# Optimization experiments

Hardware: AMD Instinct MI355X
Metric: run time of the kernel (lower is better)

The kernel has to match this reference:

```python
import jax, jax.numpy as jnp
from jax import lax
import numpy as np

B, C, FH, FW, H, V, L = 256, 512, 8, 16, 512, 64, 24


def setup_inputs() -> dict:
    key = jax.random.key(0)
    ks = jax.random.split(key, 32)
    s = 0.05
    n = lambda k, shp: jax.random.normal(k, shp, dtype=jnp.float32) * s
    return {
        "encoder_ftrs": jax.random.normal(ks[0], (B, C, FH, FW), dtype=jnp.float32),
        "sequences": jax.random.randint(ks[1], (B, L), 0, V),
        "test": 0,
        "embed_w": n(ks[2], (V, H)),
        "init_state": n(ks[3], (2, 1, H)),
        "attn_W_w": n(ks[4], (H, C)), "attn_W_b": jnp.zeros((H,), jnp.float32),
        "attn_U_w": n(ks[5], (H, H)), "attn_U_b": jnp.zeros((H,), jnp.float32),
        "attn_v_w": n(ks[6], (1, H)), "attn_v_b": jnp.zeros((1,), jnp.float32),
        "fc_w": n(ks[7], (H, C + H)), "fc_b": jnp.zeros((H,), jnp.float32),
        "cls_w": n(ks[8], (V, H)), "cls_b": jnp.zeros((V,), jnp.float32),
        "gru0_wih": n(ks[9], (3 * H, 2 * H)), "gru0_whh": n(ks[10], (3 * H, H)),
        "gru0_bih": jnp.zeros((3 * H,), jnp.float32), "gru0_bhh": jnp.zeros((3 * H,), jnp.float32),
        "gru1_wih": n(ks[11], (3 * H, H)), "gru1_whh": n(ks[12], (3 * H, H)),
        "gru1_bih": jnp.zeros((3 * H,), jnp.float32), "gru1_bhh": jnp.zeros((3 * H,), jnp.float32),
    }


def _gru_cell(x, h, wih, whh, bih, bhh):
    # PyTorch GRUCell: r,z gates then candidate n with r applied on hidden path
    gi = x @ wih.T + bih
    gh = h @ whh.T + bhh
    i_r, i_z, i_n = jnp.split(gi, 3, axis=-1)
    h_r, h_z, h_n = jnp.split(gh, 3, axis=-1)
    r = jax.nn.sigmoid(i_r + h_r)
    z = jax.nn.sigmoid(i_z + h_z)
    nact = jnp.tanh(i_n + r * h_n)
    return (1.0 - z) * nact + z * h


def reference(encoder_ftrs, sequences, test, embed_w, init_state,
              attn_W_w, attn_W_b, attn_U_w, attn_U_b, attn_v_w, attn_v_b,
              fc_w, fc_b, cls_w, cls_b,
              gru0_wih, gru0_whh, gru0_bih, gru0_bhh,
              gru1_wih, gru1_whh, gru1_bih, gru1_bhh):
    bsz = encoder_ftrs.shape[0]
    # [B, L_sp, C] encoder states
    states = encoder_ftrs.reshape(bsz, C, -1).transpose(0, 2, 1)
    # attn_W(states) is timestep-independent: precompute once (same math)
    Ws = states @ attn_W_w.T + attn_W_b  # [B, L_sp, H]

    def apply_attn(h_top):
        e = jax.nn.relu(Ws + (h_top @ attn_U_w.T + attn_U_b)[:, None, :])
        scores = e @ attn_v_w[0] + attn_v_b[0]          # [B, L_sp]
        a = jax.nn.softmax(scores, axis=-1)
        ctx = jnp.einsum('bl,blc->bc', a, states)        # [B, C]
        return ctx

    def out_proj(ctx, h_top):
        return jax.nn.relu(jnp.concatenate([ctx, h_top], axis=-1) @ fc_w.T + fc_b)

    xs = embed_w[sequences[:, :-1]]                      # [B, T, H]
    h0 = jnp.broadcast_to(init_state, (2, bsz, H))       # repeat over batch
    y0 = out_proj(apply_attn(h0[1]), h0[1])              # time_step == -1 (output dropped)

    def step(carry, x_t):
        h, y = carry
        h_l0 = _gru_cell(jnp.concatenate([y, x_t], axis=-1), h[0],
                         gru0_wih, gru0_whh, gru0_bih, gru0_bhh)
        h_l1 = _gru_cell(h_l0, h[1], gru1_wih, gru1_whh, gru1_bih, gru1_bhh)
        hn = jnp.stack([h_l0, h_l1], axis=0)
        yn = out_proj(apply_attn(h_l1), h_l1)
        return (hn, yn), yn

    _, ys = lax.scan(step, (h0, y0), xs.transpose(1, 0, 2))   # [T, B, H]
    logits = ys.transpose(1, 0, 2) @ cls_w.T + cls_b          # [B, T, V]

    labels = sequences[:, 1:]
    mask = (labels > 0).astype(logits.dtype)
    logp = jax.nn.log_softmax(logits, axis=-1)
    nll = -jnp.take_along_axis(logp, labels[..., None], axis=-1)[..., 0]
    loss = jnp.sum(nll * mask) / jnp.sum(mask)
    return loss
```

## Files before the change

kernel.cpp:

```cpp
#include <hip/hip_runtime.h>
#include <hip/hip_bf16.h>
#include <cstddef>

#define BB 256
#define CC 512
#define SS 128
#define HH 512
#define VV 64
#define LL 24

typedef unsigned short ush;
typedef __attribute__((ext_vector_type(8))) short short8;
typedef __attribute__((ext_vector_type(4))) float f32x4;

__device__ __forceinline__ float wave_sum(float v) {
#pragma unroll
    for (int off = 32; off > 0; off >>= 1) v += __shfl_xor(v, off);
    return v;
}
__device__ __forceinline__ float wave_max(float v) {
#pragma unroll
    for (int off = 32; off > 0; off >>= 1) v = fmaxf(v, __shfl_xor(v, off));
    return v;
}
__device__ __forceinline__ float sigm(float x) { return 1.0f / (1.0f + expf(-x)); }
__device__ __forceinline__ ush f2bf(float f) {
    unsigned u = __float_as_uint(f);
    u += 0x7FFFu + ((u >> 16) & 1u);
    return (ush)(u >> 16);
}
__device__ __forceinline__ float bf2f(ush b) {
    return __uint_as_float(((unsigned)b) << 16);
}
__device__ __forceinline__ unsigned pack2(float a, float b) {
    return (unsigned)f2bf(a) | ((unsigned)f2bf(b) << 16);
}

__global__ __launch_bounds__(256) void init_kernel(const float* __restrict__ init_state,
                                                   float* __restrict__ h0,
                                                   float* __restrict__ h1,
                                                   ush* __restrict__ h0b,
                                                   ush* __restrict__ h1b,
                                                   float* __restrict__ acc) {
    int idx = blockIdx.x * 256 + threadIdx.x;
    if (idx < BB * HH) {
        float a = init_state[idx & (HH - 1)];
        float b = init_state[HH + (idx & (HH - 1))];
        h0[idx] = a; h1[idx] = b;
        h0b[idx] = f2bf(a); h1b[idx] = f2bf(b);
    }
    if (idx < 2) acc[idx] = 0.0f;
}

__global__ __launch_bounds__(256) void conv_kernel(const float* __restrict__ src,
                                                   ush* __restrict__ dst, int n4) {
    int i = blockIdx.x * 256 + threadIdx.x;
    if (i < n4) {
        float4 v = ((const float4*)src)[i];
        uint2 o;
        o.x = pack2(v.x, v.y);
        o.y = pack2(v.z, v.w);
        ((uint2*)dst)[i] = o;
    }
}

__global__ __launch_bounds__(128) void gather_kernel(const float* __restrict__ embed_w,
                                                     const int* __restrict__ seq,
                                                     ush* __restrict__ xall) {
    int item = blockIdx.x;
    int t = item >> 8, m = item & 255;
    int row = seq[m * LL + t];
    float4 v = ((const float4*)(embed_w + (size_t)row * HH))[threadIdx.x];
    uint2 o;
    o.x = pack2(v.x, v.y);
    o.y = pack2(v.z, v.w);
    ((uint2*)(xall + (size_t)item * HH))[threadIdx.x] = o;
}

__global__ __launch_bounds__(256) void enc_conv(const float* __restrict__ enc,
                                                ush* __restrict__ enc_t) {
    int b = blockIdx.x, cg = blockIdx.y;
    int c0 = cg * 128;
    __shared__ ush tile[128][130];
    const float* src = enc + ((size_t)b * 512 + c0) * 128;
#pragma unroll
    for (int i = 0; i < 16; i++) {
        int lin = i * 256 + threadIdx.x;
        int cl = lin >> 5, s4 = lin & 31;
        float4 v = ((const float4*)(src + (size_t)cl * 128))[s4];
        ush b0 = f2bf(v.x), b1 = f2bf(v.y), b2 = f2bf(v.z), b3 = f2bf(v.w);
        tile[s4 * 4 + 0][cl] = b0;
        tile[s4 * 4 + 1][cl] = b1;
        tile[s4 * 4 + 2][cl] = b2;
        tile[s4 * 4 + 3][cl] = b3;
    }
    __syncthreads();
#pragma unroll
    for (int i = 0; i < 16; i++) {
        int lin = i * 256 + threadIdx.x;
        int sl = lin >> 5, c4 = lin & 31;
        ush a0 = tile[sl][c4 * 4 + 0], a1 = tile[sl][c4 * 4 + 1];
        ush a2 = tile[sl][c4 * 4 + 2], a3 = tile[sl][c4 * 4 + 3];
        uint2 o;
        o.x = (unsigned)a0 | ((unsigned)a1 << 16);
        o.y = (unsigned)a2 | ((unsigned)a3 << 16);
        ((uint2*)(enc_t + ((size_t)b * 128 + sl) * 512 + c0))[c4] = o;
    }
}

__global__ __launch_bounds__(256) void ws_v2(const ush* __restrict__ enc_t,
                                             const ush* __restrict__ Wb,
                                             const float* __restrict__ bias,
                                             ush* __restrict__ Ws_bf) {
    int tid = threadIdx.x;
    int wave = tid >> 6, lane = tid & 63;
    int quad = lane >> 4, l16 = lane & 15;
    int m0 = blockIdx.x * 128 + wave * 32;
    int n0 = blockIdx.y * 128;
    const ush* ap = enc_t + (size_t)(m0 + l16) * 512 + quad * 8;
    const ush* bp = Wb + (size_t)(n0 + l16) * 512 + quad * 8;
    f32x4 acc[2][8];
#pragma unroll
    for (int f = 0; f < 2; f++)
#pragma unroll
        for (int s = 0; s < 8; s++) acc[f][s] = (f32x4){0.f, 0.f, 0.f, 0.f};
    short8 ac[2], bc[8], an[2], bn[8];
    ac[0] = *(const short8*)(ap);
    ac[1] = *(const short8*)(ap + (size_t)16 * 512);
#pragma unroll
    for (int s = 0; s < 8; s++) bc[s] = *(const short8*)(bp + (size_t)s * 16 * 512);
#pragma unroll
    for (int ks = 0; ks < 16; ks++) {
        if (ks < 15) {
            int k = (ks + 1) * 32;
            an[0] = *(const short8*)(ap + k);
            an[1] = *(const short8*)(ap + (size_t)16 * 512 + k);
#pragma unroll
            for (int s = 0; s < 8; s++)
                bn[s] = *(const short8*)(bp + (size_t)s * 16 * 512 + k);
        }
#pragma unroll
        for (int f = 0; f < 2; f++)
#pragma unroll
            for (int s = 0; s < 8; s++)
                acc[f][s] = __builtin_amdgcn_mfma_f32_16x16x32_bf16(ac[f], bc[s], acc[f][s], 0, 0, 0);
        if (ks < 15) {
            ac[0] = an[0]; ac[1] = an[1];
#pragma unroll
            for (int s = 0; s < 8; s++) bc[s] = bn[s];
        }
    }
#pragma unroll
    for (int s = 0; s < 8; s++) {
        int n = n0 + s * 16 + l16;
        float bs = bias[n];
#pragma unroll
        for (int f = 0; f < 2; f++)
#pragma unroll
            for (int r = 0; r < 4; r++) {
                int m = m0 + f * 16 + quad * 4 + r;
                Ws_bf[(size_t)m * HH + n] = f2bf(acc[f][s][r] + bs);
            }
    }
}

template <int NSTEP>
__device__ __forceinline__ void segk(const ush* __restrict__ ap,
                                     const ush* __restrict__ bp,
                                     size_t wofs, f32x4& a0, f32x4& a1) {
    short8 as[4], bs0[4], bs1[4];
    constexpr int PRE = NSTEP < 4 ? NSTEP : 4;
#pragma unroll
    for (int i = 0; i < PRE; i++) {
        as[i]  = *(const short8*)(ap + 32 * i);
        bs0[i] = *(const short8*)(bp + 32 * i);
        bs1[i] = *(const short8*)(bp + wofs + 32 * i);
    }
#pragma unroll
    for (int i = 0; i < NSTEP; i++) {
        const int sl = i & 3;
        a0 = __builtin_amdgcn_mfma_f32_16x16x32_bf16(as[sl], bs0[sl], a0, 0, 0, 0);
        a1 = __builtin_amdgcn_mfma_f32_16x16x32_bf16(as[sl], bs1[sl], a1, 0, 0, 0);
        if (i + 4 < NSTEP) {
            as[sl]  = *(const short8*)(ap + 32 * (i + 4));
            bs0[sl] = *(const short8*)(bp + 32 * (i + 4));
            bs1[sl] = *(const short8*)(bp + wofs + 32 * (i + 4));
        }
    }
}

struct GruArgs {
    const ush* xs[8][2];
    const ush* wb[8][2];
    int wst[8][2];
    int nks[8][2];
    int slot[8][2];
    int zmask;
};

__global__ __launch_bounds__(512) void gru_fused(GruArgs A,
                                                 const float* __restrict__ h_prev,
                                                 const float* __restrict__ bih,
                                                 const float* __restrict__ bhh,
                                                 float* __restrict__ h_out,
                                                 ush* __restrict__ h_out_bf) {
    int tid = threadIdx.x;
    int wave = __builtin_amdgcn_readfirstlane(tid >> 6);
    int lane = tid & 63, quad = lane >> 4, l16 = lane & 15;
    int m0 = blockIdx.x * 16, n0 = blockIdx.y * 32;
    __shared__ float gbuf[10][16][32];
    if (A.zmask) {
        int mi = tid >> 5, ni = tid & 31;
#pragma unroll
        for (int s = 0; s < 10; s++)
            if ((A.zmask >> s) & 1) gbuf[s][mi][ni] = 0.0f;
    }
    for (int e = 0; e < 2; e++) {
        int nks = A.nks[wave][e];
        if (nks == 0) continue;
        f32x4 a0 = (f32x4){0.f, 0.f, 0.f, 0.f};
        f32x4 a1 = (f32x4){0.f, 0.f, 0.f, 0.f};
        int wst = A.wst[wave][e];
        const ush* ap = A.xs[wave][e] + (size_t)(m0 + l16) * 512 + quad * 8;
        const ush* bp = A.wb[wave][e] + (size_t)(n0 + l16) * wst + quad * 8;
        size_t wofs = (size_t)16 * wst;
        if (nks == 16) segk<16>(ap, bp, wofs, a0, a1);
        else           segk<8>(ap, bp, wofs, a0, a1);
        int sl = A.slot[wave][e];
#pragma unroll
        for (int r = 0; r < 4; r++) {
            gbuf[sl][quad * 4 + r][l16]      = a0[r];
            gbuf[sl][quad * 4 + r][16 + l16] = a1[r];
        }
    }
    __syncthreads();
    {
        int mi = tid >> 5, ni = tid & 31;
        int n = n0 + ni;
        size_t off = (size_t)(m0 + mi) * HH + n;
        float r  = sigm(gbuf[0][mi][ni] + gbuf[1][mi][ni] + gbuf[2][mi][ni] +
                        bih[n] + bhh[n]);
        float zf = sigm(gbuf[3][mi][ni] + gbuf[4][mi][ni] + gbuf[5][mi][ni] +
                        bih[512 + n] + bhh[512 + n]);
        float na = tanhf(gbuf[6][mi][ni] + gbuf[7][mi][ni] + bih[1024 + n] +
                         r * (gbuf[8][mi][ni] + gbuf[9][mi][ni] + bhh[1024 + n]));
        float hp = h_prev[off];
        float ho = (1.0f - zf) * na + zf * hp;
        h_out[off] = ho;
        h_out_bf[off] = f2bf(ho);
    }
}

__global__ __launch_bounds__(512) void fc_fused(const ush* __restrict__ ctx,
                                                const ush* __restrict__ h,
                                                const ush* __restrict__ wFc,
                                                const float* __restrict__ bias,
                                                ush* __restrict__ y,
                                                ush* __restrict__ ys) {
    int tid = threadIdx.x;
    int wave = __builtin_amdgcn_readfirstlane(tid >> 6);
    int lane = tid & 63, quad = lane >> 4, l16 = lane & 15;
    int m0 = blockIdx.x * 16, n0 = blockIdx.y * 32;
    const ush* X = (wave < 4) ? ctx : h;
    int q = wave & 3;
    f32x4 a0 = (f32x4){0.f, 0.f, 0.f, 0.f};
    f32x4 a1 = (f32x4){0.f, 0.f, 0.f, 0.f};
    const ush* ap = X + (size_t)(m0 + l16) * 512 + q * 128 + quad * 8;
    const ush* bp = wFc + (size_t)(n0 + l16) * 1024 + (wave >= 4 ? 512 : 0) + q * 128 + quad * 8;
    segk<4>(ap, bp, (size_t)16 * 1024, a0, a1);
    __shared__ float gbuf[8][16][32];
#pragma unroll
    for (int r = 0; r < 4; r++) {
        gbuf[wave][quad * 4 + r][l16]      = a0[r];
        gbuf[wave][quad * 4 + r][16 + l16] = a1[r];
    }
    __syncthreads();
    {
        int mi = tid >> 5, ni = tid & 31;
        int n = n0 + ni;
        float v = bias[n];
#pragma unroll
        for (int w = 0; w < 8; w++) v += gbuf[w][mi][ni];
        v = fmaxf(v, 0.0f);
        ush bb = f2bf(v);
        size_t off = (size_t)(m0 + mi) * HH + n;
        y[off] = bb;
        if (ys) ys[off] = bb;
    }
}

__global__ __launch_bounds__(512) void u_fused(const ush* __restrict__ h,
                                               const ush* __restrict__ wU,
                                               const float* __restrict__ Ub,
                                               float* __restrict__ Uo) {
    int tid = threadIdx.x;
    int wave = __builtin_amdgcn_readfirstlane(tid >> 6);
    int lane = tid & 63, quad = lane >> 4, l16 = lane & 15;
    int m0 = blockIdx.x * 16, n0 = blockIdx.y * 32;
    f32x4 a0 = (f32x4){0.f, 0.f, 0.f, 0.f};
    f32x4 a1 = (f32x4){0.f, 0.f, 0.f, 0.f};
    const ush* ap = h + (size_t)(m0 + l16) * 512 + wave * 64 + quad * 8;
    const ush* bp = wU + (size_t)(n0 + l16) * 512 + wave * 64 + quad * 8;
    segk<2>(ap, bp, (size_t)16 * 512, a0, a1);
    __shared__ float gbuf[8][16][32];
#pragma unroll
    for (int r = 0; r < 4; r++) {
        gbuf[wave][quad * 4 + r][l16]      = a0[r];
        gbuf[wave][quad * 4 + r][16 + l16] = a1[r];
    }
    __syncthreads();
    {
        int mi = tid >> 5, ni = tid & 31;
        int n = n0 + ni;
        float v = Ub[n];
#pragma unroll
        for (int w = 0; w < 8; w++) v += gbuf[w][mi][ni];
        Uo[(size_t)(m0 + mi) * HH + n] = v;
    }
}

__global__ __launch_bounds__(512) void attn3(const float* __restrict__ u,
                                             const float* __restrict__ vw,
                                             const ush* __restrict__ Ws_bf,
                                             const ush* __restrict__ enc_t,
                                             ush* __restrict__ ctx_bf) {
    int b = blockIdx.x;
    int tid = threadIdx.x;
    int wave = tid >> 6, lane = tid & 63;
    int hi = lane >> 4, li = lane & 15;
    __shared__ float a[SS];
    __shared__ float part[8][512];

    float ur[4][8], vr[4][8];
#pragma unroll
    for (int p = 0; p < 4; p++) {
        const float* up = u + (size_t)b * HH + p * 128 + li * 8;
        const float* vp = vw + p * 128 + li * 8;
        float4 u0 = *(const float4*)(up);
        float4 u1 = *(const float4*)(up + 4);
        float4 v0 = *(const float4*)(vp);
        float4 v1 = *(const float4*)(vp + 4);
        ur[p][0] = u0.x; ur[p][1] = u0.y; ur[p][2] = u0.z; ur[p][3] = u0.w;
        ur[p][4] = u1.x; ur[p][5] = u1.y; ur[p][6] = u1.z; ur[p][7] = u1.w;
        vr[p][0] = v0.x; vr[p][1] = v0.y; vr[p][2] = v0.z; vr[p][3] = v0.w;
        vr[p][4] = v1.x; vr[p][5] = v1.y; vr[p][6] = v1.z; vr[p][7] = v1.w;
    }
    const ush* wsb = Ws_bf + (size_t)b * SS * HH;
#pragma unroll
    for (int pass = 0; pass < 4; pass++) {
        int s = pass * 32 + wave * 4 + hi;
        float acc = 0.0f;
#pragma unroll
        for (int p = 0; p < 4; p++) {
            short8 rv = *(const short8*)(wsb + (size_t)s * HH + p * 128 + li * 8);
#pragma unroll
            for (int j = 0; j < 8; j++) {
                float e = bf2f((ush)rv[j]) + ur[p][j];
                acc += fmaxf(e, 0.0f) * vr[p][j];
            }
        }
#pragma unroll
        for (int off = 1; off < 16; off <<= 1) acc += __shfl_xor(acc, off);
        if (li == 0) a[s] = acc;
    }
    __syncthreads();
    if (wave == 0) {
        float s0v = a[lane], s1v = a[lane + 64];
        float m = wave_max(fmaxf(s0v, s1v));
        float e0 = expf(s0v - m), e1 = expf(s1v - m);
        float ssum = wave_sum(e0 + e1);
        float inv = 1.0f / ssum;
        a[lane] = e0 * inv;
        a[lane + 64] = e1 * inv;
    }
    __syncthreads();
    float c8[8];
#pragma unroll
    for (int j = 0; j < 8; j++) c8[j] = 0.0f;
    const ush* ebt = enc_t + (size_t)b * SS * 512;
#pragma unroll
    for (int i = 0; i < 16; i++) {
        int s = wave * 16 + i;
        float as = a[s];
        short8 ev = *(const short8*)(ebt + (size_t)s * 512 + lane * 8);
#pragma unroll
        for (int j = 0; j < 8; j++) c8[j] += as * bf2f((ush)ev[j]);
    }
    *(float4*)(&part[wave][lane * 8])     = (float4){c8[0], c8[1], c8[2], c8[3]};
    *(float4*)(&part[wave][lane * 8 + 4]) = (float4){c8[4], c8[5], c8[6], c8[7]};
    __syncthreads();
    {
        float sum = 0.0f;
#pragma unroll
        for (int w = 0; w < 8; w++) sum += part[w][tid];
        ctx_bf[(size_t)b * CC + tid] = f2bf(sum);
    }
}

__global__ __launch_bounds__(256) void cls_fused(const ush* __restrict__ ys,
                                                 const ush* __restrict__ wCls,
                                                 const float* __restrict__ cls_b,
                                                 const int* __restrict__ seq,
                                                 float* __restrict__ acc) {
    int tid = threadIdx.x;
    int wave = tid >> 6, lane = tid & 63;
    int quad = lane >> 4, l16 = lane & 15;
    int m0 = blockIdx.x * 16;
    f32x4 a4[4];
#pragma unroll
    for (int s = 0; s < 4; s++) a4[s] = (f32x4){0.f, 0.f, 0.f, 0.f};
    const ush* ap = ys + (size_t)(m0 + l16) * 512 + wave * 128 + quad * 8;
    const ush* bp = wCls + (size_t)l16 * 512 + wave * 128 + quad * 8;
#pragma unroll
    for (int ks = 0; ks < 4; ks++) {
        short8 av = *(const short8*)(ap + ks * 32);
#pragma unroll
        for (int s = 0; s < 4; s++) {
            short8 bv = *(const short8*)(bp + (size_t)s * 16 * 512 + ks * 32);
            a4[s] = __builtin_amdgcn_mfma_f32_16x16x32_bf16(av, bv, a4[s], 0, 0, 0);
        }
    }
    __shared__ float gbuf[4][16][64];
    __shared__ float red[8];
#pragma unroll
    for (int s = 0; s < 4; s++)
#pragma unroll
        for (int r = 0; r < 4; r++)
            gbuf[wave][quad * 4 + r][s * 16 + l16] = a4[s][r];
    __syncthreads();
    float lsum = 0.0f, lcnt = 0.0f;
#pragma unroll
    for (int ii = 0; ii < 4; ii++) {
        int mi = wave * 4 + ii;
        int item = m0 + mi;
        int t = item >> 8, b = item & 255;
        float v = gbuf[0][mi][lane] + gbuf[1][mi][lane] + gbuf[2][mi][lane] +
                  gbuf[3][mi][lane] + cls_b[lane];
        float mx = wave_max(v);
        float e = expf(v - mx);
        float ssum = wave_sum(e);
        int label = seq[b * LL + t + 1];
        float vl = __shfl(v, label);
        if (label > 0) {
            lsum += -(vl - mx - logf(ssum));
            lcnt += 1.0f;
        }
    }
    if (lane == 0) { red[wave] = lsum; red[4 + wave] = lcnt; }
    __syncthreads();
    if (tid == 0) {
        atomicAdd(&acc[0], red[0] + red[1] + red[2] + red[3]);
        atomicAdd(&acc[1], red[4] + red[5] + red[6] + red[7]);
    }
}

__global__ void final_kernel(const float* __restrict__ acc, float* __restrict__ out) {
    if (threadIdx.x == 0) out[0] = acc[0] / acc[1];
}

extern "C" void kernel_launch(void* const* d_in, const int* in_sizes, int n_in,
                              void* d_out, int out_size, void* d_ws, size_t ws_size,
                              hipStream_t stream) {
    const float* enc        = (const float*)d_in[0];
    const int*   seq        = (const int*)d_in[1];
    const float* embed_w    = (const float*)d_in[3];
    const float* init_state = (const float*)d_in[4];
    const float* attn_W_w   = (const float*)d_in[5];
    const float* attn_W_b   = (const float*)d_in[6];
    const float* attn_U_w   = (const float*)d_in[7];
    const float* attn_U_b   = (const float*)d_in[8];
    const float* attn_v_w   = (const float*)d_in[9];
    const float* fc_w       = (const float*)d_in[11];
    const float* fc_b       = (const float*)d_in[12];
    const float* cls_w      = (const float*)d_in[13];
    const float* cls_b      = (const float*)d_in[14];
    const float* g0_wih     = (const float*)d_in[15];
    const float* g0_whh     = (const float*)d_in[16];
    const float* g0_bih     = (const float*)d_in[17];
    const float* g0_bhh     = (const float*)d_in[18];
    const float* g1_wih     = (const float*)d_in[19];
    const float* g1_whh     = (const float*)d_in[20];
    const float* g1_bih     = (const float*)d_in[21];
    const float* g1_bhh     = (const float*)d_in[22];
    float* out = (float*)d_out;

    float* ws = (float*)d_ws;
    size_t o = 0;
    ush* Ws_bf   = (ush*)(ws + o); o += (size_t)BB * SS * HH / 2;
    ush* enc_t   = (ush*)(ws + o); o += (size_t)BB * CC * SS / 2;
    ush* ys_bf   = (ush*)(ws + o); o += (size_t)(LL - 1) * BB * HH / 2;
    ush* xall_bf = (ush*)(ws + o); o += (size_t)(LL - 1) * BB * HH / 2;
    ush* wWb  = (ush*)(ws + o); o += 262144 / 2;
    ush* wU   = (ush*)(ws + o); o += 262144 / 2;
    ush* wFc  = (ush*)(ws + o); o += 524288 / 2;
    ush* wCls = (ush*)(ws + o); o += 32768 / 2;
    ush* wG0i = (ush*)(ws + o); o += 1572864 / 2;
    ush* wG0h = (ush*)(ws + o); o += 786432 / 2;
    ush* wG1i = (ush*)(ws + o); o += 786432 / 2;
    ush* wG1h = (ush*)(ws + o); o += 786432 / 2;
    float* Uo   = ws + o; o += (size_t)BB * HH;
    float* h0a  = ws + o; o += (size_t)BB * HH;
    float* h0b  = ws + o; o += (size_t)BB * HH;
    float* h1a  = ws + o; o += (size_t)BB * HH;
    float* h1b  = ws + o; o += (size_t)BB * HH;
    float* acc  = ws + o; o += 256;
    ush* h0a_bf = (ush*)(ws + o); o += (size_t)BB * HH / 2;
    ush* h0b_bf = (ush*)(ws + o); o += (size_t)BB * HH / 2;
    ush* h1a_bf = (ush*)(ws + o); o += (size_t)BB * HH / 2;
    ush* h1b_bf = (ush*)(ws + o); o += (size_t)BB * HH / 2;
    ush* y_bf   = (ush*)(ws + o); o += (size_t)BB * HH / 2;
    ush* ctx_bf = (ush*)(ws + o); o += (size_t)BB * CC / 2;

    init_kernel<<<512, 256, 0, stream>>>(init_state, h0a, h1a, h0a_bf, h1a_bf, acc);
    conv_kernel<<<256, 256, 0, stream>>>(attn_W_w, wWb, 65536);
    conv_kernel<<<256, 256, 0, stream>>>(attn_U_w, wU, 65536);
    conv_kernel<<<512, 256, 0, stream>>>(fc_w, wFc, 131072);
    conv_kernel<<<32, 256, 0, stream>>>(cls_w, wCls, 8192);
    conv_kernel<<<1536, 256, 0, stream>>>(g0_wih, wG0i, 393216);
    conv_kernel<<<768, 256, 0, stream>>>(g0_whh, wG0h, 196608);
    conv_kernel<<<768, 256, 0, stream>>>(g1_wih, wG1i, 196608);
    conv_kernel<<<768, 256, 0, stream>>>(g1_whh, wG1h, 196608);
    enc_conv<<<dim3(256, 4), 256, 0, stream>>>(enc, enc_t);
    gather_kernel<<<(LL - 1) * BB, 128, 0, stream>>>(embed_w, seq, xall_bf);
    ws_v2<<<dim3(256, 4), 256, 0, stream>>>(enc_t, wWb, attn_W_b, Ws_bf);

    auto setw = [](GruArgs& a, int w, int e, const ush* xs, const ush* wb,
                   int wst, int nks, int slot) {
        a.xs[w][e] = xs; a.wb[w][e] = wb; a.wst[w][e] = wst;
        a.nks[w][e] = nks; a.slot[w][e] = slot;
    };
    auto gru0_args = [&](const ush* y, const ush* x, const ush* h0) {
        GruArgs a{};
        setw(a, 0, 0, y,        wG0i,                             1024, 16, 0);
        setw(a, 1, 0, x,        wG0i + 512,                       1024, 16, 1);
        setw(a, 2, 0, h0,       wG0h,                              512, 16, 2);
        setw(a, 3, 0, y,        wG0i + (size_t)512 * 1024,        1024, 16, 3);
        setw(a, 4, 0, x,        wG0i + (size_t)512 * 1024 + 512,  1024, 16, 4);
        setw(a, 5, 0, h0,       wG0h + (size_t)512 * 512,          512, 16, 5);
        setw(a, 6, 0, y,        wG0i + (size_t)1024 * 1024,       1024, 16, 6);
        setw(a, 7, 0, x,        wG0i + (size_t)1024 * 1024 + 512, 1024, 16, 7);
        setw(a, 6, 1, h0,       wG0h + (size_t)1024 * 512,         512,  8, 8);
        setw(a, 7, 1, h0 + 256, wG0h + (size_t)1024 * 512 + 256,   512,  8, 9);
        a.zmask = 0;
        return a;
    };
    auto gru1_args = [&](const ush* hl0, const ush* h1) {
        GruArgs a{};
        setw(a, 0, 0, hl0,       wG1i,                             512, 16, 0);
        setw(a, 1, 0, h1,        wG1h,                             512, 16, 1);
        setw(a, 2, 0, hl0,       wG1i + (size_t)512 * 512,         512, 16, 3);
        setw(a, 3, 0, h1,        wG1h + (size_t)512 * 512,         512, 16, 4);
        setw(a, 4, 0, hl0,       wG1i + (size_t)1024 * 512,        512,  8, 6);
        setw(a, 5, 0, hl0 + 256, wG1i + (size_t)1024 * 512 + 256,  512,  8, 7);
        setw(a, 6, 0, h1,        wG1h + (size_t)1024 * 512,        512,  8, 8);
        setw(a, 7, 0, h1 + 256,  wG1h + (size_t)1024 * 512 + 256,  512,  8, 9);
        a.zmask = (1 << 2) | (1 << 5);
        return a;
    };

    u_fused<<<dim3(16, 16), 512, 0, stream>>>(h1a_bf, wU, attn_U_b, Uo);
    attn3<<<BB, 512, 0, stream>>>(Uo, attn_v_w, Ws_bf, enc_t, ctx_bf);
    fc_fused<<<dim3(16, 16), 512, 0, stream>>>(ctx_bf, h1a_bf, wFc, fc_b, y_bf, nullptr);

    float* h0_in = h0a; float* h0_out = h0b;
    float* h1_in = h1a; float* h1_out = h1b;
    ush* h0_in_bf = h0a_bf; ush* h0_out_bf = h0b_bf;
    ush* h1_in_bf = h1a_bf; ush* h1_out_bf = h1b_bf;
    for (int t = 0; t < LL - 1; t++) {
        gru_fused<<<dim3(16, 16), 512, 0, stream>>>(
            gru0_args(y_bf, xall_bf + (size_t)t * BB * HH, h0_in_bf),
            h0_in, g0_bih, g0_bhh, h0_out, h0_out_bf);
        gru_fused<<<dim3(16, 16), 512, 0, stream>>>(
            gru1_args(h0_out_bf, h1_in_bf),
            h1_in, g1_bih, g1_bhh, h1_out, h1_out_bf);
        u_fused<<<dim3(16, 16), 512, 0, stream>>>(h1_out_bf, wU, attn_U_b, Uo);
        attn3<<<BB, 512, 0, stream>>>(Uo, attn_v_w, Ws_bf, enc_t, ctx_bf);
        fc_fused<<<dim3(16, 16), 512, 0, stream>>>(ctx_bf, h1_out_bf, wFc, fc_b,
                                                   y_bf, ys_bf + (size_t)t * BB * HH);
        float* tmp;
        tmp = h0_in; h0_in = h0_out; h0_out = tmp;
        tmp = h1_in; h1_in = h1_out; h1_out = tmp;
        ush* tb;
        tb = h0_in_bf; h0_in_bf = h0_out_bf; h0_out_bf = tb;
        tb = h1_in_bf; h1_in_bf = h1_out_bf; h1_out_bf = tb;
    }

    cls_fused<<<368, 256, 0, stream>>>(ys_bf, wCls, cls_b, seq, acc);
    final_kernel<<<1, 1, 0, stream>>>(acc, out);
}
```

Before: 1.395 ms.

## Merge weight conversions into one launch and compute Ws directly from fp32 encoder

```diff
diff --git a/kernel.cpp b/kernel.cpp
--- a/kernel.cpp
+++ b/kernel.cpp
@@ -52,16 +52,22 @@
     if (idx < 2) acc[idx] = 0.0f;
 }
 
-__global__ __launch_bounds__(256) void conv_kernel(const float* __restrict__ src,
-                                                   ush* __restrict__ dst, int n4) {
-    int i = blockIdx.x * 256 + threadIdx.x;
-    if (i < n4) {
-        float4 v = ((const float4*)src)[i];
-        uint2 o;
-        o.x = pack2(v.x, v.y);
-        o.y = pack2(v.z, v.w);
-        ((uint2*)dst)[i] = o;
-    }
+struct CvArgs {
+    const float* src[8];
+    ush* dst[8];
+    int end[8];
+};
+__global__ __launch_bounds__(256) void conv_multi(CvArgs A) {
+    int blk = blockIdx.x;
+    int s = 0;
+    while (s < 7 && blk >= A.end[s]) s++;
+    int base = s ? A.end[s - 1] : 0;
+    int i = (blk - base) * 256 + threadIdx.x;
+    float4 v = ((const float4*)A.src[s])[i];
+    uint2 o;
+    o.x = pack2(v.x, v.y);
+    o.y = pack2(v.z, v.w);
+    ((uint2*)A.dst[s])[i] = o;
 }
 
 __global__ __launch_bounds__(128) void gather_kernel(const float* __restrict__ embed_w,
@@ -88,11 +94,10 @@
         int lin = i * 256 + threadIdx.x;
         int cl = lin >> 5, s4 = lin & 31;
         float4 v = ((const float4*)(src + (size_t)cl * 128))[s4];
-        ush b0 = f2bf(v.x), b1 = f2bf(v.y), b2 = f2bf(v.z), b3 = f2bf(v.w);
-        tile[s4 * 4 + 0][cl] = b0;
-        tile[s4 * 4 + 1][cl] = b1;
-        tile[s4 * 4 + 2][cl] = b2;
-        tile[s4 * 4 + 3][cl] = b3;
+        tile[s4 * 4 + 0][cl] = f2bf(v.x);
+        tile[s4 * 4 + 1][cl] = f2bf(v.y);
+        tile[s4 * 4 + 2][cl] = f2bf(v.z);
+        tile[s4 * 4 + 3][cl] = f2bf(v.w);
     }
     __syncthreads();
 #pragma unroll
@@ -108,60 +113,54 @@
     }
 }
 
-__global__ __launch_bounds__(256) void ws_v2(const ush* __restrict__ enc_t,
-                                             const ush* __restrict__ Wb,
-                                             const float* __restrict__ bias,
-                                             ush* __restrict__ Ws_bf) {
+__global__ __launch_bounds__(256) void ws_mfma(const float* __restrict__ enc,
+                                               const ush* __restrict__ Wb,
+                                               const float* __restrict__ bias,
+                                               ush* __restrict__ Ws_bf) {
     int tid = threadIdx.x;
     int wave = tid >> 6, lane = tid & 63;
     int quad = lane >> 4, l16 = lane & 15;
-    int m0 = blockIdx.x * 128 + wave * 32;
-    int n0 = blockIdx.y * 128;
-    const ush* ap = enc_t + (size_t)(m0 + l16) * 512 + quad * 8;
-    const ush* bp = Wb + (size_t)(n0 + l16) * 512 + quad * 8;
-    f32x4 acc[2][8];
-#pragma unroll
-    for (int f = 0; f < 2; f++)
-#pragma unroll
-        for (int s = 0; s < 8; s++) acc[f][s] = (f32x4){0.f, 0.f, 0.f, 0.f};
-    short8 ac[2], bc[8], an[2], bn[8];
-    ac[0] = *(const short8*)(ap);
-    ac[1] = *(const short8*)(ap + (size_t)16 * 512);
-#pragma unroll
-    for (int s = 0; s < 8; s++) bc[s] = *(const short8*)(bp + (size_t)s * 16 * 512);
-#pragma unroll
-    for (int ks = 0; ks < 16; ks++) {
-        if (ks < 15) {
-            int k = (ks + 1) * 32;
-            an[0] = *(const short8*)(ap + k);
-            an[1] = *(const short8*)(ap + (size_t)16 * 512 + k);
-#pragma unroll
-            for (int s = 0; s < 8; s++)
-                bn[s] = *(const short8*)(bp + (size_t)s * 16 * 512 + k);
+    int m0 = blockIdx.x * 256 + wave * 64;
+    int n0 = blockIdx.y * 64;
+    int b = m0 >> 7;
+    int s_base = m0 & 127;
+    const float* eb = enc + (size_t)b * CC * SS;
+    const ush* wp = Wb + (size_t)(n0 + l16) * 512 + quad * 8;
+    f32x4 acc[4][4];
+#pragma unroll
+    for (int f = 0; f < 4; f++)
+#pragma unroll
+        for (int s = 0; s < 4; s++) acc[f][s] = (f32x4){0.f, 0.f, 0.f, 0.f};
+    for (int k0 = 0; k0 < 512; k0 += 32) {
+        short8 af[4], bfr[4];
+#pragma unroll
+        for (int f = 0; f < 4; f++) {
+            int s = s_base + f * 16 + l16;
+#pragma unroll
+            for (int j = 0; j < 8; j++) {
+                float v = eb[(size_t)(k0 + quad * 8 + j) * SS + s];
+                af[f][j] = (short)f2bf(v);
+            }
         }
 #pragma unroll
-        for (int f = 0; f < 2; f++)
-#pragma unroll
-            for (int s = 0; s < 8; s++)
-                acc[f][s] = __builtin_amdgcn_mfma_f32_16x16x32_bf16(ac[f], bc[s], acc[f][s], 0, 0, 0);
-        if (ks < 15) {
-            ac[0] = an[0]; ac[1] = an[1];
-#pragma unroll
-            for (int s = 0; s < 8; s++) bc[s] = bn[s];
-        }
-    }
-#pragma unroll
-    for (int s = 0; s < 8; s++) {
-        int n = n0 + s * 16 + l16;
-        float bs = bias[n];
-#pragma unroll
-        for (int f = 0; f < 2; f++)
+        for (int s = 0; s < 4; s++)
+            bfr[s] = *(const short8*)(wp + (size_t)s * 16 * 512 + k0);
+#pragma unroll
+        for (int f = 0; f < 4; f++)
+#pragma unroll
+            for (int s = 0; s < 4; s++)
+                acc[f][s] = __builtin_amdgcn_mfma_f32_16x16x32_bf16(af[f], bfr[s], acc[f][s], 0, 0, 0);
+    }
+#pragma unroll
+    for (int f = 0; f < 4; f++)
+#pragma unroll
+        for (int s = 0; s < 4; s++)
 #pragma unroll
             for (int r = 0; r < 4; r++) {
                 int m = m0 + f * 16 + quad * 4 + r;
-                Ws_bf[(size_t)m * HH + n] = f2bf(acc[f][s][r] + bs);
+                int n = n0 + s * 16 + l16;
+                Ws_bf[(size_t)m * HH + n] = f2bf(acc[f][s][r] + bias[n]);
             }
-    }
 }
 
 template <int NSTEP>
@@ -210,7 +209,7 @@
     int m0 = blockIdx.x * 16, n0 = blockIdx.y * 32;
     __shared__ float gbuf[10][16][32];
     if (A.zmask) {
-        int mi = tid >> 5, ni = tid & 31;
+        int mi = (tid >> 5) & 15, ni = tid & 31;
 #pragma unroll
         for (int s = 0; s < 10; s++)
             if ((A.zmask >> s) & 1) gbuf[s][mi][ni] = 0.0f;
@@ -512,17 +511,23 @@
     ush* ctx_bf = (ush*)(ws + o); o += (size_t)BB * CC / 2;
 
     init_kernel<<<512, 256, 0, stream>>>(init_state, h0a, h1a, h0a_bf, h1a_bf, acc);
-    conv_kernel<<<256, 256, 0, stream>>>(attn_W_w, wWb, 65536);
-    conv_kernel<<<256, 256, 0, stream>>>(attn_U_w, wU, 65536);
-    conv_kernel<<<512, 256, 0, stream>>>(fc_w, wFc, 131072);
-    conv_kernel<<<32, 256, 0, stream>>>(cls_w, wCls, 8192);
-    conv_kernel<<<1536, 256, 0, stream>>>(g0_wih, wG0i, 393216);
-    conv_kernel<<<768, 256, 0, stream>>>(g0_whh, wG0h, 196608);
-    conv_kernel<<<768, 256, 0, stream>>>(g1_wih, wG1i, 196608);
-    conv_kernel<<<768, 256, 0, stream>>>(g1_whh, wG1h, 196608);
+    {
+        CvArgs cv{};
+        cv.src[0] = attn_W_w; cv.dst[0] = wWb;
+        cv.src[1] = attn_U_w; cv.dst[1] = wU;
+        cv.src[2] = fc_w;     cv.dst[2] = wFc;
+        cv.src[3] = cls_w;    cv.dst[3] = wCls;
+        cv.src[4] = g0_wih;   cv.dst[4] = wG0i;
+        cv.src[5] = g0_whh;   cv.dst[5] = wG0h;
+        cv.src[6] = g1_wih;   cv.dst[6] = wG1i;
+        cv.src[7] = g1_whh;   cv.dst[7] = wG1h;
+        cv.end[0] = 256;  cv.end[1] = 512;  cv.end[2] = 1024; cv.end[3] = 1056;
+        cv.end[4] = 2592; cv.end[5] = 3360; cv.end[6] = 4128; cv.end[7] = 4896;
+        conv_multi<<<4896, 256, 0, stream>>>(cv);
+    }
     enc_conv<<<dim3(256, 4), 256, 0, stream>>>(enc, enc_t);
     gather_kernel<<<(LL - 1) * BB, 128, 0, stream>>>(embed_w, seq, xall_bf);
-    ws_v2<<<dim3(256, 4), 256, 0, stream>>>(enc_t, wWb, attn_W_b, Ws_bf);
+    ws_mfma<<<dim3(128, 8), 256, 0, stream>>>(enc, wWb, attn_W_b, Ws_bf);
 
     auto setw = [](GruArgs& a, int w, int e, const ush* xs, const ush* wb,
                    int wst, int nks, int slot) {
```

Result: faster. 1.368 ms (-2.0%).
